# Kernel optimization log

Hardware: AMD Instinct MI355X
Metric: run time of the kernel (lower is better)

## Reference

```python
import jax, jax.numpy as jnp
import numpy as np

B, S, K, N = 4, 2048, 4096, 4096


def setup_inputs() -> dict:
    key = jax.random.key(0)
    k1, k2, k3, k4 = jax.random.split(key, 4)
    x = jax.random.normal(k1, (B, S, K), dtype=jnp.float32)
    # int8 quantized weight values in [-128, 127], stored as int32 (jax-friendly container)
    qw = jax.random.randint(k2, (N, K), -128, 128, dtype=jnp.int32)
    # per-tensor scale: amax/127 style scalar
    sw = (jax.random.uniform(k3, (), dtype=jnp.float32) * 0.02 + 0.001)
    bias = jax.random.normal(k4, (N,), dtype=jnp.float32)
    return {"x": x, "qw": qw, "sw": sw, "bias": bias}


def reference(x, qw, sw, bias):
    # per_tensor_matmul: dequantize weight to fp32 with scalar scale, fp32 GEMM, cast back, add bias
    x_dtype = x.dtype
    w = qw.astype(jnp.float32) * sw          # [N, K] dequantized
    y = jnp.einsum('bsk,nk->bsn', x.astype(jnp.float32), w).astype(x_dtype)
    y = y + bias                              # [B, S, N]
    return y
```

## Files before the change

### kernel.cpp

```cpp
#include <hip/hip_runtime.h>
#include <stdint.h>

#define MDIM 8192
#define NDIM 4096
#define KDIM 4096

#define BM 256
#define BN 256
#define BK 128
#define NKT (KDIM / BK)

typedef __attribute__((ext_vector_type(4)))  int i32x4;
typedef __attribute__((ext_vector_type(16))) int i32x16;

#define AS1 __attribute__((address_space(1)))
#define AS3 __attribute__((address_space(3)))

__device__ __forceinline__ int clamp127(int v) {
    return v > 127 ? 127 : (v < -127 ? -127 : v);
}

__global__ __launch_bounds__(256) void quant_x(
        const float* __restrict__ x, const float* __restrict__ sw,
        int8_t* __restrict__ Aq, float* __restrict__ scales) {
    const int row = blockIdx.x;
    const int t   = threadIdx.x;
    const float4* px = (const float4*)(x + (size_t)row * KDIM);

    float4 v[4];
#pragma unroll
    for (int j = 0; j < 4; j++) v[j] = px[t + 256 * j];

    float a = 0.f;
#pragma unroll
    for (int j = 0; j < 4; j++) {
        a = fmaxf(a, fabsf(v[j].x)); a = fmaxf(a, fabsf(v[j].y));
        a = fmaxf(a, fabsf(v[j].z)); a = fmaxf(a, fabsf(v[j].w));
    }
#pragma unroll
    for (int off = 32; off >= 1; off >>= 1)
        a = fmaxf(a, __shfl_xor(a, off));
    __shared__ float red[4];
    if ((t & 63) == 0) red[t >> 6] = a;
    __syncthreads();
    const float amax = fmaxf(fmaxf(red[0], red[1]), fmaxf(red[2], red[3]));
    const float inv  = (amax > 0.f) ? (127.0f / amax) : 0.f;
    if (t == 0) scales[row] = (amax * (1.0f / 127.0f)) * (*sw);

    int* out32 = (int*)(Aq + (size_t)row * KDIM);
#pragma unroll
    for (int j = 0; j < 4; j++) {
        int b0 = clamp127(__float2int_rn(v[j].x * inv));
        int b1 = clamp127(__float2int_rn(v[j].y * inv));
        int b2 = clamp127(__float2int_rn(v[j].z * inv));
        int b3 = clamp127(__float2int_rn(v[j].w * inv));
        out32[t + 256 * j] = (b0 & 255) | ((b1 & 255) << 8) | ((b2 & 255) << 16) | ((b3 & 255) << 24);
    }
}

__global__ __launch_bounds__(256) void cvt_w(const int* __restrict__ qw, int8_t* __restrict__ Bq) {
    const long i = (long)blockIdx.x * 256 + threadIdx.x;
    int4 a = ((const int4*)qw)[i];
    ((int*)Bq)[i] = (a.x & 255) | ((a.y & 255) << 8) | ((a.z & 255) << 16) | ((a.w & 255) << 24);
}


#define BAR()   do { asm volatile("" ::: "memory"); __builtin_amdgcn_s_barrier(); asm volatile("" ::: "memory"); } while (0)
#define LGKM0() asm volatile("s_waitcnt lgkmcnt(0)" ::: "memory")
#define WAITV(n) asm volatile("s_waitcnt vmcnt(" #n ")" ::: "memory")

#define STAGE_A(buf, h, kt) do { \
    __builtin_amdgcn_global_load_lds((AS1 const void*)(gA + (size_t)((h) * 128) * KDIM + (kt) * 128), \
        (AS3 void*)(sA + (buf) * 32768 + (h) * 16384 + sdst), 16, 0, 0); \
    __builtin_amdgcn_global_load_lds((AS1 const void*)(gA + (size_t)((h) * 128 + 64) * KDIM + (kt) * 128), \
        (AS3 void*)(sA + (buf) * 32768 + (h) * 16384 + 8192 + sdst), 16, 0, 0); \
} while (0)

#define STAGE_B(buf, h, kt) do { \
    __builtin_amdgcn_global_load_lds((AS1 const void*)(gB + (size_t)((h) * 128) * KDIM + (kt) * 128), \
        (AS3 void*)(sB + (buf) * 32768 + (h) * 16384 + sdst), 16, 0, 0); \
    __builtin_amdgcn_global_load_lds((AS1 const void*)(gB + (size_t)((h) * 128 + 64) * KDIM + (kt) * 128), \
        (AS3 void*)(sB + (buf) * 32768 + (h) * 16384 + 8192 + sdst), 16, 0, 0); \
} while (0)

#define READ_A(buf, mh) do { \
    _Pragma("unroll") for (int q = 0; q < 2; ++q) \
    _Pragma("unroll") for (int ks = 0; ks < 4; ++ks) \
        aF[q][ks] = *(const i32x4*)(sA + (buf) * 32768 + rbA + ((mh) * 2 + q) * 4096 + co[ks]); \
} while (0)

#define READ_B(buf, ni) do { \
    _Pragma("unroll") for (int ks = 0; ks < 4; ++ks) \
        bF[ni][ks] = *(const i32x4*)(sB + (buf) * 32768 + rbB + (ni) * 4096 + co[ks]); \
} while (0)

#define MMA(mh, ni) do { \
    __builtin_amdgcn_s_setprio(1); \
    _Pragma("unroll") for (int ks = 0; ks < 4; ++ks) { \
        acc[(mh) * 2][ni]     = __builtin_amdgcn_mfma_i32_32x32x32_i8(aF[0][ks], bF[ni][ks], acc[(mh) * 2][ni], 0, 0, 0); \
        acc[(mh) * 2 + 1][ni] = __builtin_amdgcn_mfma_i32_32x32x32_i8(aF[1][ks], bF[ni][ks], acc[(mh) * 2 + 1][ni], 0, 0, 0); \
    } \
    __builtin_amdgcn_s_setprio(0); \
} while (0)

__global__ __launch_bounds__(512, 2) void gemm_bt_i8(
        const int8_t* __restrict__ A,
        const int8_t* __restrict__ Bm,
        const float* __restrict__ scales,
        const float* __restrict__ bias,
        float* __restrict__ C)
{
    __shared__ __align__(16) int8_t sA[2 * BM * BK];
    __shared__ __align__(16) int8_t sB[2 * BN * BK];

    const int tid  = threadIdx.x;
    const int wave = tid >> 6;
    const int lane = tid & 63;
    const int wr   = wave >> 2;
    const int wc   = wave & 3;
    const int l32  = lane & 31;
    const int hi   = lane >> 5;

    const int orig = blockIdx.y * 16 + blockIdx.x;
    const int nu   = (orig & 7) * 64 + (orig >> 3);
    const int m0   = (nu >> 4) * BM;
    const int n0   = (nu & 15) * BN;

    const int trow = tid >> 3;
    const int slog = (tid & 7) ^ (trow & 7);
    const int8_t* gA = A  + (size_t)(m0 + trow) * KDIM + slog * 16;
    const int8_t* gB = Bm + (size_t)(n0 + trow) * KDIM + slog * 16;
    const int sdst = tid * 16;

    const int swz = l32 & 7;
    const int rbA = (wr * 128 + l32) * BK;
    const int rbB = (wc * 64  + l32) * BK;
    int co[4];
#pragma unroll
    for (int ks = 0; ks < 4; ++ks) co[ks] = ((((ks << 1) | hi) ^ swz) << 4);

    i32x16 acc[4][2];
#pragma unroll
    for (int mi = 0; mi < 4; ++mi)
#pragma unroll
        for (int ni = 0; ni < 2; ++ni)
#pragma unroll
            for (int r = 0; r < 16; ++r) acc[mi][ni][r] = 0;

    i32x4 aF[2][4];
    i32x4 bF[2][4];

    STAGE_B(0, 0, 0); STAGE_B(0, 1, 0);
    STAGE_A(0, 0, 0); STAGE_A(0, 1, 0);
    STAGE_B(1, 0, 1); STAGE_B(1, 1, 1);
    WAITV(4);
    BAR();

#pragma unroll 1
    for (int it = 0; it < NKT / 2 - 1; ++it) {
        const int t1 = 2 * it + 1, t2 = 2 * it + 2, t3 = 2 * it + 3;
        READ_A(0, 0); READ_B(0, 0); STAGE_A(1, 0, t1); BAR(); LGKM0(); MMA(0, 0); BAR();
        READ_B(0, 1);               STAGE_A(1, 1, t1); BAR(); LGKM0(); MMA(0, 1); BAR();
        READ_A(0, 1);               STAGE_B(0, 0, t2); BAR(); LGKM0(); MMA(1, 1); BAR();
        STAGE_B(0, 1, t2); WAITV(4); BAR();                           MMA(1, 0); BAR();
        READ_A(1, 0); READ_B(1, 0); STAGE_A(0, 0, t2); BAR(); LGKM0(); MMA(0, 0); BAR();
        READ_B(1, 1);               STAGE_A(0, 1, t2); BAR(); LGKM0(); MMA(0, 1); BAR();
        READ_A(1, 1);               STAGE_B(1, 0, t3); BAR(); LGKM0(); MMA(1, 1); BAR();
        STAGE_B(1, 1, t3); WAITV(4); BAR();                           MMA(1, 0); BAR();
    }

    READ_A(0, 0); READ_B(0, 0); STAGE_A(1, 0, 31); BAR(); LGKM0(); MMA(0, 0); BAR();
    READ_B(0, 1);               STAGE_A(1, 1, 31); BAR(); LGKM0(); MMA(0, 1); BAR();
    READ_A(0, 1);                                  BAR(); LGKM0(); MMA(1, 1); BAR();
    WAITV(0); BAR();                                                MMA(1, 0); BAR();
    READ_A(1, 0); READ_B(1, 0);                    BAR(); LGKM0(); MMA(0, 0); BAR();
    READ_B(1, 1);                                  BAR(); LGKM0(); MMA(0, 1); BAR();
    READ_A(1, 1);                                         LGKM0(); MMA(1, 1);
    MMA(1, 0);

#pragma unroll
    for (int mi = 0; mi < 4; ++mi) {
        const int row_base = m0 + wr * 128 + mi * 32 + 4 * hi;
        float sc[16];
#pragma unroll
        for (int r = 0; r < 16; ++r)
            sc[r] = scales[row_base + (r & 3) + 8 * (r >> 2)];
#pragma unroll
        for (int ni = 0; ni < 2; ++ni) {
            const int col = n0 + wc * 64 + ni * 32 + l32;
            const float bc = bias[col];
#pragma unroll
            for (int r = 0; r < 16; ++r) {
                const int row = row_base + (r & 3) + 8 * (r >> 2);
                C[(size_t)row * NDIM + col] = (float)acc[mi][ni][r] * sc[r] + bc;
            }
        }
    }
}

__global__ void gemm_naive_f32(const float* __restrict__ x, const int* __restrict__ qw,
                               const float* __restrict__ sw, const float* __restrict__ bias,
                               float* __restrict__ out) {
    size_t id = (size_t)blockIdx.x * blockDim.x + threadIdx.x;
    if (id >= (size_t)MDIM * NDIM) return;
    int m = (int)(id / NDIM);
    int n = (int)(id % NDIM);
    const float* xr = x + (size_t)m * KDIM;
    const int*   wr = qw + (size_t)n * KDIM;
    float acc = 0.f;
    for (int k = 0; k < KDIM; k++) acc += xr[k] * (float)wr[k];
    out[id] = acc * (*sw) + bias[n];
}

extern "C" void kernel_launch(void* const* d_in, const int* in_sizes, int n_in,
                              void* d_out, int out_size, void* d_ws, size_t ws_size,
                              hipStream_t stream) {
    const float* x    = (const float*)d_in[0];
    const int*   qw   = (const int*)d_in[1];
    const float* sw   = (const float*)d_in[2];
    const float* bias = (const float*)d_in[3];
    float* out = (float*)d_out;

    const size_t needA = (size_t)MDIM * KDIM;
    const size_t needB = (size_t)NDIM * KDIM;
    const size_t needS = (size_t)MDIM * sizeof(float);

    if (ws_size >= needA + needB + needS) {
        int8_t* Aq = (int8_t*)d_ws;
        int8_t* Bq = Aq + needA;
        float*  scales = (float*)(Bq + needB);

        quant_x<<<MDIM, 256, 0, stream>>>(x, sw, Aq, scales);
        const long nw4 = (long)NDIM * KDIM / 4;
        cvt_w<<<(int)(nw4 / 256), 256, 0, stream>>>(qw, Bq);

        dim3 grid(NDIM / BN, MDIM / BM);
        gemm_bt_i8<<<grid, 512, 0, stream>>>(Aq, Bq, scales, bias, out);
    } else {
        size_t total = (size_t)MDIM * NDIM;
        gemm_naive_f32<<<(total + 255) / 256, 256, 0, stream>>>(x, qw, sw, bias, out);
    }
}
```

Measured before the change: 404.6 us.

## Restructure int8 GEMM main loop with separate A fragment registers and compiler-managed LDS waits

```diff
diff --git a/kernel.cpp b/kernel.cpp
--- a/kernel.cpp
+++ b/kernel.cpp
@@ -65,8 +65,7 @@
 }
 
 
-#define BAR()   do { asm volatile("" ::: "memory"); __builtin_amdgcn_s_barrier(); asm volatile("" ::: "memory"); } while (0)
-#define LGKM0() asm volatile("s_waitcnt lgkmcnt(0)" ::: "memory")
+#define BAR()    do { asm volatile("" ::: "memory"); __builtin_amdgcn_s_barrier(); asm volatile("" ::: "memory"); } while (0)
 #define WAITV(n) asm volatile("s_waitcnt vmcnt(" #n ")" ::: "memory")
 
 #define STAGE_A(buf, h, kt) do { \
@@ -83,22 +82,38 @@
         (AS3 void*)(sB + (buf) * 32768 + (h) * 16384 + 8192 + sdst), 16, 0, 0); \
 } while (0)
 
-#define READ_A(buf, mh) do { \
+#define READ_A0(buf) do { \
     _Pragma("unroll") for (int q = 0; q < 2; ++q) \
     _Pragma("unroll") for (int ks = 0; ks < 4; ++ks) \
-        aF[q][ks] = *(const i32x4*)(sA + (buf) * 32768 + rbA + ((mh) * 2 + q) * 4096 + co[ks]); \
-} while (0)
-
-#define READ_B(buf, ni) do { \
+        aF0[q][ks] = *(const i32x4*)(sA + (buf) * 32768 + rbA + q * 4096 + co[ks]); \
+} while (0)
+
+#define READ_A1(buf) do { \
+    _Pragma("unroll") for (int q = 0; q < 2; ++q) \
+    _Pragma("unroll") for (int ks = 0; ks < 4; ++ks) \
+        aF1[q][ks] = *(const i32x4*)(sA + (buf) * 32768 + rbA + (2 + q) * 4096 + co[ks]); \
+} while (0)
+
+#define READ_Bb(buf) do { \
+    _Pragma("unroll") for (int ni = 0; ni < 2; ++ni) \
     _Pragma("unroll") for (int ks = 0; ks < 4; ++ks) \
         bF[ni][ks] = *(const i32x4*)(sB + (buf) * 32768 + rbB + (ni) * 4096 + co[ks]); \
 } while (0)
 
-#define MMA(mh, ni) do { \
+#define MMA0(ni) do { \
     __builtin_amdgcn_s_setprio(1); \
     _Pragma("unroll") for (int ks = 0; ks < 4; ++ks) { \
-        acc[(mh) * 2][ni]     = __builtin_amdgcn_mfma_i32_32x32x32_i8(aF[0][ks], bF[ni][ks], acc[(mh) * 2][ni], 0, 0, 0); \
-        acc[(mh) * 2 + 1][ni] = __builtin_amdgcn_mfma_i32_32x32x32_i8(aF[1][ks], bF[ni][ks], acc[(mh) * 2 + 1][ni], 0, 0, 0); \
+        acc[0][ni] = __builtin_amdgcn_mfma_i32_32x32x32_i8(aF0[0][ks], bF[ni][ks], acc[0][ni], 0, 0, 0); \
+        acc[1][ni] = __builtin_amdgcn_mfma_i32_32x32x32_i8(aF0[1][ks], bF[ni][ks], acc[1][ni], 0, 0, 0); \
+    } \
+    __builtin_amdgcn_s_setprio(0); \
+} while (0)
+
+#define MMA1(ni) do { \
+    __builtin_amdgcn_s_setprio(1); \
+    _Pragma("unroll") for (int ks = 0; ks < 4; ++ks) { \
+        acc[2][ni] = __builtin_amdgcn_mfma_i32_32x32x32_i8(aF1[0][ks], bF[ni][ks], acc[2][ni], 0, 0, 0); \
+        acc[3][ni] = __builtin_amdgcn_mfma_i32_32x32x32_i8(aF1[1][ks], bF[ni][ks], acc[3][ni], 0, 0, 0); \
     } \
     __builtin_amdgcn_s_setprio(0); \
 } while (0)
@@ -147,36 +162,39 @@
 #pragma unroll
             for (int r = 0; r < 16; ++r) acc[mi][ni][r] = 0;
 
-    i32x4 aF[2][4];
+    i32x4 aF0[2][4];
+    i32x4 aF1[2][4];
     i32x4 bF[2][4];
 
     STAGE_B(0, 0, 0); STAGE_B(0, 1, 0);
     STAGE_A(0, 0, 0); STAGE_A(0, 1, 0);
     STAGE_B(1, 0, 1); STAGE_B(1, 1, 1);
-    WAITV(4);
+    STAGE_A(1, 0, 1); STAGE_A(1, 1, 1);
+    WAITV(8);
     BAR();
 
 #pragma unroll 1
     for (int it = 0; it < NKT / 2 - 1; ++it) {
-        const int t1 = 2 * it + 1, t2 = 2 * it + 2, t3 = 2 * it + 3;
-        READ_A(0, 0); READ_B(0, 0); STAGE_A(1, 0, t1); BAR(); LGKM0(); MMA(0, 0); BAR();
-        READ_B(0, 1);               STAGE_A(1, 1, t1); BAR(); LGKM0(); MMA(0, 1); BAR();
-        READ_A(0, 1);               STAGE_B(0, 0, t2); BAR(); LGKM0(); MMA(1, 1); BAR();
-        STAGE_B(0, 1, t2); WAITV(4); BAR();                           MMA(1, 0); BAR();
-        READ_A(1, 0); READ_B(1, 0); STAGE_A(0, 0, t2); BAR(); LGKM0(); MMA(0, 0); BAR();
-        READ_B(1, 1);               STAGE_A(0, 1, t2); BAR(); LGKM0(); MMA(0, 1); BAR();
-        READ_A(1, 1);               STAGE_B(1, 0, t3); BAR(); LGKM0(); MMA(1, 1); BAR();
-        STAGE_B(1, 1, t3); WAITV(4); BAR();                           MMA(1, 0); BAR();
-    }
-
-    READ_A(0, 0); READ_B(0, 0); STAGE_A(1, 0, 31); BAR(); LGKM0(); MMA(0, 0); BAR();
-    READ_B(0, 1);               STAGE_A(1, 1, 31); BAR(); LGKM0(); MMA(0, 1); BAR();
-    READ_A(0, 1);                                  BAR(); LGKM0(); MMA(1, 1); BAR();
-    WAITV(0); BAR();                                                MMA(1, 0); BAR();
-    READ_A(1, 0); READ_B(1, 0);                    BAR(); LGKM0(); MMA(0, 0); BAR();
-    READ_B(1, 1);                                  BAR(); LGKM0(); MMA(0, 1); BAR();
-    READ_A(1, 1);                                         LGKM0(); MMA(1, 1);
-    MMA(1, 0);
+        const int t2 = 2 * it + 2, t3 = 2 * it + 3;
+        READ_A0(0); READ_Bb(0);                    BAR(); MMA0(0); BAR();
+        READ_A1(0);                                BAR(); MMA0(1); BAR();
+        STAGE_B(0, 0, t2);                         BAR(); MMA1(1); BAR();
+        STAGE_B(0, 1, t2); WAITV(4);               BAR(); MMA1(0); BAR();
+        READ_A0(1); READ_Bb(1);
+        STAGE_A(0, 0, t2); STAGE_A(0, 1, t2);      BAR(); MMA0(0); BAR();
+        READ_A1(1);                                BAR(); MMA0(1); BAR();
+        STAGE_B(1, 0, t3); STAGE_B(1, 1, t3);      BAR(); MMA1(1); BAR();
+        STAGE_A(1, 0, t3); STAGE_A(1, 1, t3); WAITV(8); BAR(); MMA1(0); BAR();
+    }
+
+    READ_A0(0); READ_Bb(0);                        BAR(); MMA0(0); BAR();
+    READ_A1(0);                                    BAR(); MMA0(1); BAR();
+                                                   BAR(); MMA1(1); BAR();
+    WAITV(0);                                      BAR(); MMA1(0); BAR();
+    READ_A0(1); READ_Bb(1);                        BAR(); MMA0(0); BAR();
+    READ_A1(1);                                    BAR(); MMA0(1); BAR();
+    MMA1(1);
+    MMA1(0);
 
 #pragma unroll
     for (int mi = 0; mi < 4; ++mi) {
```

Result: no change. 406.7 us (+0.5%).
